# Kernel optimization log

Hardware: AMD Instinct MI355X
Metric: run time of the kernel (lower is better)

## Reference

```python
import jax, jax.numpy as jnp
import numpy as np

BS, SEQ, H = 8, 2048, 1024   # batch, tokens, hidden (longformer-large)
NSP = 32                     # discourse spans per essay
NH, HD = 16, 64              # attention heads, head dim
MAXPOS = 512                 # BertConfig default max_position_embeddings
NLAB = 3                     # effectiveness classes
EPS = 1e-5
SCALE = float(1.0 / np.sqrt(HD))


def _layer_norm(x, g, b):
    m = jnp.mean(x, -1, keepdims=True)
    v = jnp.var(x, -1, keepdims=True)
    return (x - m) * jax.lax.rsqrt(v + EPS) * g + b


def _lstm_dir(x, Wih, Whh, b, reverse):
    # x: [B,T,D] -> [B,T,Hh]; PyTorch gate order i,f,g,o
    pre = jnp.swapaxes(x, 0, 1) @ Wih.T + b  # [T,B,4Hh] input projection precomputed
    Hh = Whh.shape[1]
    z = jnp.zeros((x.shape[0], Hh), x.dtype)

    def step(carry, p):
        h, c = carry
        gates = p + h @ Whh.T
        i, f, g, o = jnp.split(gates, 4, axis=-1)
        c = jax.nn.sigmoid(f) * c + jax.nn.sigmoid(i) * jnp.tanh(g)
        h = jax.nn.sigmoid(o) * jnp.tanh(c)
        return (h, c), h

    _, ys = jax.lax.scan(step, (z, z), pre, reverse=reverse)
    return jnp.swapaxes(ys, 0, 1)


def _forward(span_head_idxs, span_tail_idxs, encoder_layer, span_attention_mask,
             lstm_Wih_f, lstm_Whh_f, lstm_b_f, lstm_Wih_b, lstm_Whh_b, lstm_b_b,
             ln_g, ln_b, Wq, bq, Wk, bk, Wv, bv, dist_emb, Wo, bo, ao_g, ao_b, Wc, bc):
    # BiLSTM over token features
    fwd = _lstm_dir(encoder_layer, lstm_Wih_f, lstm_Whh_f, lstm_b_f, False)
    bwd = _lstm_dir(encoder_layer, lstm_Wih_b, lstm_Whh_b, lstm_b_b, True)
    seq = jnp.concatenate([fwd, bwd], -1)  # [B,S,H]
    # ragged span mean pooling over tokens in (head, tail) (head excluded)
    pos = jnp.arange(SEQ)
    m = ((pos[None, None, :] > span_head_idxs[:, :, None]) &
         (pos[None, None, :] < span_tail_idxs[:, :, None])).astype(seq.dtype)  # [B,N,S]
    cnt = jnp.sum(m, -1, keepdims=True)
    mean_vec = jnp.einsum('bns,bsd->bnd', m, seq) / cnt
    x = _layer_norm(mean_vec, ln_g, ln_b)  # [B,N,H]
    # relative-key BertAttention over spans
    sh = lambda t: jnp.swapaxes(t.reshape(BS, NSP, NH, HD), 1, 2)  # [B,NH,N,HD]
    q, k, v = sh(x @ Wq + bq), sh(x @ Wk + bk), sh(x @ Wv + bv)
    scores = jnp.einsum('bhqd,bhkd->bhqk', q, k)
    dist = jnp.arange(NSP)[:, None] - jnp.arange(NSP)[None, :] + MAXPOS - 1
    pe = dist_emb[dist]  # [N,N,HD]
    scores = (scores + jnp.einsum('bhld,lrd->bhlr', q, pe)) * SCALE
    amask = (1.0 - span_attention_mask)[:, None, None, :] * -10000.0
    probs = jax.nn.softmax(scores + amask, axis=-1)
    ctx = jnp.swapaxes(jnp.einsum('bhqk,bhkd->bhqd', probs, v), 1, 2).reshape(BS, NSP, H)
    attn_out = _layer_norm(ctx @ Wo + bo + x, ao_g, ao_b)  # BertSelfOutput residual LN
    return attn_out @ Wc + bc  # logits [B,N,NLAB]


def setup_inputs():
    key = jax.random.key(0)
    ks = jax.random.split(key, 16)
    s, Hh = 0.02, H // 2
    span_len = SEQ // NSP
    heads = jnp.tile(jnp.arange(NSP) * span_len, (BS, 1)).astype(jnp.int32)
    f32 = jnp.float32
    return dict(
        encoder_layer=jax.random.normal(ks[0], (BS, SEQ, H), f32),
        span_head_idxs=heads,
        span_tail_idxs=heads + span_len,
        span_attention_mask=jnp.ones((BS, NSP), f32),
        lstm_Wih_f=jax.random.normal(ks[1], (4 * Hh, H), f32) * s,
        lstm_Whh_f=jax.random.normal(ks[2], (4 * Hh, Hh), f32) * s,
        lstm_b_f=jnp.zeros((4 * Hh,), f32),
        lstm_Wih_b=jax.random.normal(ks[3], (4 * Hh, H), f32) * s,
        lstm_Whh_b=jax.random.normal(ks[4], (4 * Hh, Hh), f32) * s,
        lstm_b_b=jnp.zeros((4 * Hh,), f32),
        ln_g=jnp.ones((H,), f32), ln_b=jnp.zeros((H,), f32),
        Wq=jax.random.normal(ks[5], (H, H), f32) * s, bq=jnp.zeros((H,), f32),
        Wk=jax.random.normal(ks[6], (H, H), f32) * s, bk=jnp.zeros((H,), f32),
        Wv=jax.random.normal(ks[7], (H, H), f32) * s, bv=jnp.zeros((H,), f32),
        dist_emb=jax.random.normal(ks[8], (2 * MAXPOS - 1, HD), f32) * s,
        Wo=jax.random.normal(ks[9], (H, H), f32) * s, bo=jnp.zeros((H,), f32),
        ao_g=jnp.ones((H,), f32), ao_b=jnp.zeros((H,), f32),
        Wc=jax.random.normal(ks[10], (H, NLAB), f32) * s, bc=jnp.zeros((NLAB,), f32),
    )


def reference(encoder_layer, span_head_idxs, span_tail_idxs, span_attention_mask,
              lstm_Wih_f, lstm_Whh_f, lstm_b_f, lstm_Wih_b, lstm_Whh_b, lstm_b_b,
              ln_g, ln_b, Wq, bq, Wk, bk, Wv, bv, dist_emb, Wo, bo, ao_g, ao_b, Wc, bc):
    return _forward(span_head_idxs, span_tail_idxs, encoder_layer, span_attention_mask,
                    lstm_Wih_f, lstm_Whh_f, lstm_b_f, lstm_Wih_b, lstm_Whh_b, lstm_b_b,
                    ln_g, ln_b, Wq, bq, Wk, bk, Wv, bv, dist_emb, Wo, bo, ao_g, ao_b, Wc, bc)
```

## Files before the change

kernel.cpp:

```cpp
#include <hip/hip_runtime.h>
#include <hip/hip_bf16.h>

#define BSZ   8
#define SEQL  2048
#define HID   1024
#define HH    512
#define NSP   32
#define NHEAD 16
#define HDIM  64

__device__ __forceinline__ float bf2f(unsigned short u) {
    unsigned int x = ((unsigned int)u) << 16;
    return __uint_as_float(x);
}
__device__ __forceinline__ unsigned short f2bf(float f) {
    unsigned int x = __float_as_uint(f);
    unsigned int r = (x + 0x7fffu + ((x >> 16) & 1u)) >> 16;
    return (unsigned short)r;
}

__device__ __forceinline__ void ldcg4x4(const float* p0, const float* p1,
                                        const float* p2, const float* p3,
                                        float4& a, float4& b, float4& c, float4& d) {
    asm volatile(
        "global_load_dwordx4 %0, %4, off sc0 sc1\n"
        "global_load_dwordx4 %1, %5, off sc0 sc1\n"
        "global_load_dwordx4 %2, %6, off sc0 sc1\n"
        "global_load_dwordx4 %3, %7, off sc0 sc1\n"
        "s_waitcnt vmcnt(0)"
        : "=&v"(a), "=&v"(b), "=&v"(c), "=&v"(d)
        : "v"(p0), "v"(p1), "v"(p2), "v"(p3)
        : "memory");
}
__device__ __forceinline__ void stcg_wait(float* p, float v) {
    asm volatile("global_store_dword %0, %1, off sc0 sc1\n"
                 "s_waitcnt vmcnt(0)"
                 :: "v"(p), "v"(v) : "memory");
}
__device__ __forceinline__ void stcg_i(int* p, int v) {
    asm volatile("global_store_dword %0, %1, off sc0 sc1"
                 :: "v"(p), "v"(v) : "memory");
}
__device__ __forceinline__ int ldcg_i(const int* p) {
    int v;
    asm volatile("global_load_dword %0, %1, off sc0 sc1\n"
                 "s_waitcnt vmcnt(0)"
                 : "=&v"(v) : "v"(p) : "memory");
    return v;
}

template<int TB, int OUTBF16, int PERM>
__global__ __launch_bounds__(256)
void gemm_f32(const float* __restrict__ X, const float* __restrict__ W,
              const float* __restrict__ bias, void* __restrict__ out,
              int M, int N, int K)
{
    __shared__ float a_s[16][132];
    __shared__ float b_s[16][132];
    const int tid = threadIdx.x;
    const int n0 = blockIdx.x * 128;
    const int m0 = blockIdx.y * 128;
    const int tx = tid & 15, ty = tid >> 4;
    float acc[8][8];
#pragma unroll
    for (int i = 0; i < 8; i++)
#pragma unroll
        for (int j = 0; j < 8; j++) acc[i][j] = 0.f;

    for (int k0 = 0; k0 < K; k0 += 16) {
#pragma unroll
        for (int i = 0; i < 2; i++) {
            int f4 = tid + 256 * i;
            int row = f4 >> 2, kc = f4 & 3;
            float4 v = *(const float4*)(X + (size_t)(m0 + row) * K + (k0 + kc * 4));
            a_s[kc*4+0][row] = v.x; a_s[kc*4+1][row] = v.y;
            a_s[kc*4+2][row] = v.z; a_s[kc*4+3][row] = v.w;
        }
        if (TB) {
#pragma unroll
            for (int i = 0; i < 2; i++) {
                int f4 = tid + 256 * i;
                int col = f4 >> 2, kc = f4 & 3;
                float4 v = *(const float4*)(W + (size_t)(n0 + col) * K + (k0 + kc * 4));
                b_s[kc*4+0][col] = v.x; b_s[kc*4+1][col] = v.y;
                b_s[kc*4+2][col] = v.z; b_s[kc*4+3][col] = v.w;
            }
        } else {
#pragma unroll
            for (int i = 0; i < 2; i++) {
                int f4 = tid + 256 * i;
                int kk = f4 >> 5, c4 = f4 & 31;
                float4 v = *(const float4*)(W + (size_t)(k0 + kk) * N + (n0 + c4 * 4));
                b_s[kk][c4*4+0] = v.x; b_s[kk][c4*4+1] = v.y;
                b_s[kk][c4*4+2] = v.z; b_s[kk][c4*4+3] = v.w;
            }
        }
        __syncthreads();
#pragma unroll
        for (int kk = 0; kk < 16; kk++) {
            float4 af0 = *(const float4*)&a_s[kk][ty * 8];
            float4 af1 = *(const float4*)&a_s[kk][ty * 8 + 4];
            float4 bf0 = *(const float4*)&b_s[kk][tx * 8];
            float4 bf1 = *(const float4*)&b_s[kk][tx * 8 + 4];
            float af[8] = {af0.x, af0.y, af0.z, af0.w, af1.x, af1.y, af1.z, af1.w};
            float bf[8] = {bf0.x, bf0.y, bf0.z, bf0.w, bf1.x, bf1.y, bf1.z, bf1.w};
#pragma unroll
            for (int i = 0; i < 8; i++)
#pragma unroll
                for (int j = 0; j < 8; j++)
                    acc[i][j] = fmaf(af[i], bf[j], acc[i][j]);
        }
        __syncthreads();
    }
#pragma unroll
    for (int i = 0; i < 8; i++) {
        int row = m0 + ty * 8 + i;
#pragma unroll
        for (int j = 0; j < 8; j++) {
            int col = n0 + tx * 8 + j;
            float v = acc[i][j] + bias[col];
            size_t oidx;
            if (PERM) {
                int bb = row >> 11; int tt = row & 2047;
                oidx = ((size_t)tt * 8 + bb) * (size_t)N + col;
            } else {
                oidx = (size_t)row * N + col;
            }
            if (OUTBF16) ((unsigned short*)out)[oidx] = f2bf(v);
            else         ((float*)out)[oidx] = v;
        }
    }
}

__global__ __launch_bounds__(256)
void lstm_rec_kernel(const unsigned short* __restrict__ pre_f,
                     const unsigned short* __restrict__ pre_b,
                     const float* __restrict__ Whh_f,
                     const float* __restrict__ Whh_b,
                     float* __restrict__ hbuf,
                     int* __restrict__ flags,
                     unsigned short* __restrict__ seq)
{
    const int tid = threadIdx.x;
    const int d = blockIdx.x >> 6;
    const int g = blockIdx.x & 63;
    const unsigned short* pre = d ? pre_b : pre_f;
    const float* Whh = d ? Whh_b : Whh_f;
    float* hb = hbuf + (size_t)d * 2 * 8 * 512;
    int* flg = flags + d * 64 * 32;
    int* myflag = flg + g * 32;

    __shared__ float h_s[4096];
    __shared__ float gate_s[8][33];

    const int m2 = tid >> 4;
    const int tk = tid & 15;
    float wA[32], wB[32];
    {
        const int mA = m2, mB = m2 + 16;
        const int growA = (mA >> 3) * 512 + g * 8 + (mA & 7);
        const int growB = (mB >> 3) * 512 + g * 8 + (mB & 7);
#pragma unroll
        for (int qq = 0; qq < 8; qq++) {
            float4 va = *(const float4*)(Whh + (size_t)growA * 512 + (qq * 16 + tk) * 4);
            float4 vb = *(const float4*)(Whh + (size_t)growB * 512 + (qq * 16 + tk) * 4);
            wA[qq*4+0] = va.x; wA[qq*4+1] = va.y; wA[qq*4+2] = va.z; wA[qq*4+3] = va.w;
            wB[qq*4+0] = vb.x; wB[qq*4+1] = vb.y; wB[qq*4+2] = vb.z; wB[qq*4+3] = vb.w;
        }
    }
    const int ub = tid >> 3;
    const int uj = tid & 7;
    const int ujj = g * 8 + uj;
    float cst = 0.f;

    for (int s = 0; s < 2048; s++) {
        const int t = d ? (2047 - s) : s;
        const float* hin = hb + (size_t)(s & 1) * 4096;
        float* hout = hb + (size_t)((s + 1) & 1) * 4096;

        float pv0 = 0.f, pv1 = 0.f, pv2 = 0.f, pv3 = 0.f;
        if (tid < 64) {
            const size_t pb = ((size_t)t * 8 + ub) * 2048;
            pv0 = bf2f(pre[pb + ujj]);
            pv1 = bf2f(pre[pb + 512 + ujj]);
            pv2 = bf2f(pre[pb + 1024 + ujj]);
            pv3 = bf2f(pre[pb + 1536 + ujj]);
        }

        if (tid < 64) {
            const int* fp = flg + tid * 32;
            int guard = 0;
            while (1) {
                int f = ldcg_i(fp);
                if (__all(f >= s)) break;
                if (++guard > (1 << 22)) break;
                __builtin_amdgcn_s_sleep(1);
            }
        }
        __syncthreads();

        {
            const float* base = hin + tid * 4;
            float4 va, vb2, vc, vd2;
            ldcg4x4(base, base + 1024, base + 2048, base + 3072, va, vb2, vc, vd2);
            float4* dst = (float4*)h_s;
            dst[tid] = va; dst[tid + 256] = vb2; dst[tid + 512] = vc; dst[tid + 768] = vd2;
        }
        __syncthreads();

#pragma unroll 1
        for (int b2 = 0; b2 < 8; b2++) {
            const float4* h4 = (const float4*)(h_s + b2 * 512);
            float s0 = 0.f, s1 = 0.f;
#pragma unroll
            for (int qq = 0; qq < 8; qq++) {
                float4 hv = h4[qq * 16 + tk];
                s0 += hv.x * wA[qq*4+0] + hv.y * wA[qq*4+1] + hv.z * wA[qq*4+2] + hv.w * wA[qq*4+3];
                s1 += hv.x * wB[qq*4+0] + hv.y * wB[qq*4+1] + hv.z * wB[qq*4+2] + hv.w * wB[qq*4+3];
            }
#pragma unroll
            for (int off = 1; off < 16; off <<= 1) {
                s0 += __shfl_xor(s0, off);
                s1 += __shfl_xor(s1, off);
            }
            if (tk == 0) { gate_s[b2][m2] = s0; gate_s[b2][m2 + 16] = s1; }
        }
        __syncthreads();

        if (tid < 64) {
            float zi = gate_s[ub][uj]      + pv0;
            float zf = gate_s[ub][8 + uj]  + pv1;
            float zg = gate_s[ub][16 + uj] + pv2;
            float zo = gate_s[ub][24 + uj] + pv3;
            float gi = 1.f / (1.f + __expf(-zi));
            float gf = 1.f / (1.f + __expf(-zf));
            float go = 1.f / (1.f + __expf(-zo));
            cst = gf * cst + gi * tanhf(zg);
            float hv = go * tanhf(cst);
            seq[((size_t)ub * 2048 + t) * 1024 + d * 512 + ujj] = f2bf(hv);
            stcg_wait(hout + ub * 512 + ujj, hv);
        }
        __syncthreads();
        if (tid == 0) stcg_i(myflag, s + 1);
    }
}

__global__ __launch_bounds__(256)
void pool_ln_kernel(const unsigned short* __restrict__ seq,
                    const int* __restrict__ heads, const int* __restrict__ tails,
                    const float* __restrict__ lng, const float* __restrict__ lnb,
                    float* __restrict__ xln)
{
    const int bn = blockIdx.x;
    const int b = bn >> 5;
    const int tid = threadIdx.x;
    const int head = heads[bn], tail = tails[bn];
    float a0 = 0.f, a1 = 0.f, a2 = 0.f, a3 = 0.f;
    for (int t = head + 1; t < tail; t++) {
        const unsigned short* p = seq + ((size_t)b * 2048 + t) * 1024 + tid * 4;
        uint2 w = *(const uint2*)p;
        a0 += bf2f((unsigned short)(w.x & 0xffff));
        a1 += bf2f((unsigned short)(w.x >> 16));
        a2 += bf2f((unsigned short)(w.y & 0xffff));
        a3 += bf2f((unsigned short)(w.y >> 16));
    }
    float cnt = (float)(tail - head - 1);
    float x0 = a0 / cnt, x1 = a1 / cnt, x2 = a2 / cnt, x3 = a3 / cnt;
    float s1 = x0 + x1 + x2 + x3;
    float s2 = x0*x0 + x1*x1 + x2*x2 + x3*x3;
#pragma unroll
    for (int off = 1; off < 64; off <<= 1) { s1 += __shfl_xor(s1, off); s2 += __shfl_xor(s2, off); }
    __shared__ float red[8];
    if ((tid & 63) == 0) { int w = tid >> 6; red[w] = s1; red[4 + w] = s2; }
    __syncthreads();
    s1 = red[0] + red[1] + red[2] + red[3];
    s2 = red[4] + red[5] + red[6] + red[7];
    float m = s1 * (1.f / 1024.f);
    float var = s2 * (1.f / 1024.f) - m * m;
    float inv = rsqrtf(var + 1e-5f);
    int c = tid * 4;
    float* o = xln + (size_t)bn * 1024 + c;
    o[0] = (x0 - m) * inv * lng[c+0] + lnb[c+0];
    o[1] = (x1 - m) * inv * lng[c+1] + lnb[c+1];
    o[2] = (x2 - m) * inv * lng[c+2] + lnb[c+2];
    o[3] = (x3 - m) * inv * lng[c+3] + lnb[c+3];
}

__global__ __launch_bounds__(256)
void attn_kernel(const float* __restrict__ q, const float* __restrict__ k,
                 const float* __restrict__ v, const float* __restrict__ dist_emb,
                 const float* __restrict__ mask, float* __restrict__ ctx)
{
    __shared__ float q_s[32][65], k_s[32][65], v_s[32][65];
    __shared__ float pe_s[63][65];
    __shared__ float p_s[32][33];
    __shared__ float mk[32];
    const int tid = threadIdx.x;
    const int b = blockIdx.x >> 4, h = blockIdx.x & 15;

    for (int i = tid; i < 32 * 16; i += 256) {
        int n = i >> 4, c = (i & 15) * 4;
        const size_t base = ((size_t)(b * 32 + n)) * 1024 + h * 64 + c;
        float4 qv = *(const float4*)(q + base);
        float4 kv = *(const float4*)(k + base);
        float4 vv = *(const float4*)(v + base);
        q_s[n][c] = qv.x; q_s[n][c+1] = qv.y; q_s[n][c+2] = qv.z; q_s[n][c+3] = qv.w;
        k_s[n][c] = kv.x; k_s[n][c+1] = kv.y; k_s[n][c+2] = kv.z; k_s[n][c+3] = kv.w;
        v_s[n][c] = vv.x; v_s[n][c+1] = vv.y; v_s[n][c+2] = vv.z; v_s[n][c+3] = vv.w;
    }
    for (int i = tid; i < 63 * 16; i += 256) {
        int x = i >> 4, c = (i & 15) * 4;
        float4 pv = *(const float4*)(dist_emb + (size_t)(480 + x) * 64 + c);
        pe_s[x][c] = pv.x; pe_s[x][c+1] = pv.y; pe_s[x][c+2] = pv.z; pe_s[x][c+3] = pv.w;
    }
    if (tid < 32) mk[tid] = mask[b * 32 + tid];
    __syncthreads();

#pragma unroll
    for (int pi = 0; pi < 4; pi++) {
        int p = tid + 256 * pi;
        int l = p >> 5, r = p & 31;
        const float* qr = q_s[l];
        const float* kr = k_s[r];
        const float* pr = pe_s[l - r + 31];
        float acc = 0.f;
#pragma unroll
        for (int dd = 0; dd < 64; dd++) acc = fmaf(qr[dd], kr[dd] + pr[dd], acc);
        p_s[l][r] = acc * 0.125f + (1.f - mk[r]) * (-10000.f);
    }
    __syncthreads();
    {
        int l = tid >> 3, c = tid & 7;
        float v0 = p_s[l][c], v1 = p_s[l][c+8], v2 = p_s[l][c+16], v3 = p_s[l][c+24];
        float mx = fmaxf(fmaxf(v0, v1), fmaxf(v2, v3));
#pragma unroll
        for (int off = 1; off < 8; off <<= 1) mx = fmaxf(mx, __shfl_xor(mx, off));
        float e0 = __expf(v0 - mx), e1 = __expf(v1 - mx), e2 = __expf(v2 - mx), e3 = __expf(v3 - mx);
        float sm = e0 + e1 + e2 + e3;
#pragma unroll
        for (int off = 1; off < 8; off <<= 1) sm += __shfl_xor(sm, off);
        float inv = 1.f / sm;
        p_s[l][c] = e0 * inv; p_s[l][c+8] = e1 * inv; p_s[l][c+16] = e2 * inv; p_s[l][c+24] = e3 * inv;
    }
    __syncthreads();
    {
        int l = tid >> 3, dg = tid & 7;
        float o[8] = {0, 0, 0, 0, 0, 0, 0, 0};
#pragma unroll 4
        for (int r = 0; r < 32; r++) {
            float pv = p_s[l][r];
#pragma unroll
            for (int j = 0; j < 8; j++) o[j] = fmaf(pv, v_s[r][dg * 8 + j], o[j]);
        }
        size_t base = ((size_t)(b * 32 + l)) * 1024 + h * 64 + dg * 8;
#pragma unroll
        for (int j = 0; j < 8; j++) ctx[base + j] = o[j];
    }
}

__global__ __launch_bounds__(256)
void resid_ln_kernel(const float* __restrict__ tmp, const float* __restrict__ xln,
                     const float* __restrict__ g, const float* __restrict__ be,
                     float* __restrict__ out)
{
    const int bn = blockIdx.x;
    const int tid = threadIdx.x;
    size_t base = (size_t)bn * 1024 + tid * 4;
    float4 a = *(const float4*)(tmp + base);
    float4 r = *(const float4*)(xln + base);
    float x0 = a.x + r.x, x1 = a.y + r.y, x2 = a.z + r.z, x3 = a.w + r.w;
    float s1 = x0 + x1 + x2 + x3;
    float s2 = x0*x0 + x1*x1 + x2*x2 + x3*x3;
#pragma unroll
    for (int off = 1; off < 64; off <<= 1) { s1 += __shfl_xor(s1, off); s2 += __shfl_xor(s2, off); }
    __shared__ float red[8];
    if ((tid & 63) == 0) { int w = tid >> 6; red[w] = s1; red[4 + w] = s2; }
    __syncthreads();
    s1 = red[0] + red[1] + red[2] + red[3];
    s2 = red[4] + red[5] + red[6] + red[7];
    float m = s1 * (1.f / 1024.f);
    float var = s2 * (1.f / 1024.f) - m * m;
    float inv = rsqrtf(var + 1e-5f);
    int c = tid * 4;
    out[base + 0] = (x0 - m) * inv * g[c+0] + be[c+0];
    out[base + 1] = (x1 - m) * inv * g[c+1] + be[c+1];
    out[base + 2] = (x2 - m) * inv * g[c+2] + be[c+2];
    out[base + 3] = (x3 - m) * inv * g[c+3] + be[c+3];
}

__global__ __launch_bounds__(256)
void classify_kernel(const float* __restrict__ x, const float* __restrict__ Wc,
                     const float* __restrict__ bc, float* __restrict__ out)
{
    const int bn = blockIdx.x;
    const int tid = threadIdx.x;
    const float* row = x + (size_t)bn * 1024;
    float a0 = 0.f, a1 = 0.f, a2 = 0.f;
    for (int kk = tid; kk < 1024; kk += 256) {
        float xv = row[kk];
        a0 = fmaf(xv, Wc[kk * 3 + 0], a0);
        a1 = fmaf(xv, Wc[kk * 3 + 1], a1);
        a2 = fmaf(xv, Wc[kk * 3 + 2], a2);
    }
#pragma unroll
    for (int off = 1; off < 64; off <<= 1) {
        a0 += __shfl_xor(a0, off); a1 += __shfl_xor(a1, off); a2 += __shfl_xor(a2, off);
    }
    __shared__ float red[12];
    if ((tid & 63) == 0) { int w = tid >> 6; red[w*3] = a0; red[w*3+1] = a1; red[w*3+2] = a2; }
    __syncthreads();
    if (tid == 0) {
        out[bn * 3 + 0] = red[0] + red[3] + red[6] + red[9]  + bc[0];
        out[bn * 3 + 1] = red[1] + red[4] + red[7] + red[10] + bc[1];
        out[bn * 3 + 2] = red[2] + red[5] + red[8] + red[11] + bc[2];
    }
}

#define OFF_PREF 0ull
#define OFF_PREB 67108864ull
#define OFF_SEQ  134217728ull
#define OFF_XLN  167772160ull
#define OFF_Q    168820736ull
#define OFF_K    169869312ull
#define OFF_V    170917888ull
#define OFF_CTX  171966464ull
#define OFF_TMP  173015040ull
#define OFF_ATT  174063616ull
#define OFF_HBUF 175112192ull
#define OFF_SYNC 175177728ull

extern "C" void kernel_launch(void* const* d_in, const int* in_sizes, int n_in,
                              void* d_out, int out_size, void* d_ws, size_t ws_size,
                              hipStream_t stream)
{
    const float* enc   = (const float*)d_in[0];
    const int*   heads = (const int*)d_in[1];
    const int*   tails = (const int*)d_in[2];
    const float* amask = (const float*)d_in[3];
    const float* Wih_f = (const float*)d_in[4];
    const float* Whh_f = (const float*)d_in[5];
    const float* b_f   = (const float*)d_in[6];
    const float* Wih_b = (const float*)d_in[7];
    const float* Whh_b = (const float*)d_in[8];
    const float* b_b   = (const float*)d_in[9];
    const float* ln_g  = (const float*)d_in[10];
    const float* ln_b  = (const float*)d_in[11];
    const float* Wq    = (const float*)d_in[12];
    const float* bq    = (const float*)d_in[13];
    const float* Wk    = (const float*)d_in[14];
    const float* bk    = (const float*)d_in[15];
    const float* Wv    = (const float*)d_in[16];
    const float* bv    = (const float*)d_in[17];
    const float* dist  = (const float*)d_in[18];
    const float* Wo    = (const float*)d_in[19];
    const float* bo    = (const float*)d_in[20];
    const float* ao_g  = (const float*)d_in[21];
    const float* ao_b  = (const float*)d_in[22];
    const float* Wc    = (const float*)d_in[23];
    const float* bc    = (const float*)d_in[24];

    char* ws = (char*)d_ws;
    unsigned short* pre_f = (unsigned short*)(ws + OFF_PREF);
    unsigned short* pre_b = (unsigned short*)(ws + OFF_PREB);
    unsigned short* seqp  = (unsigned short*)(ws + OFF_SEQ);
    float* xlnp = (float*)(ws + OFF_XLN);
    float* qb   = (float*)(ws + OFF_Q);
    float* kb   = (float*)(ws + OFF_K);
    float* vb   = (float*)(ws + OFF_V);
    float* ctxb = (float*)(ws + OFF_CTX);
    float* tmpb = (float*)(ws + OFF_TMP);
    float* attb = (float*)(ws + OFF_ATT);
    float* hbuf = (float*)(ws + OFF_HBUF);
    int*   flags = (int*)(ws + OFF_SYNC);

    hipMemsetAsync(ws + OFF_HBUF, 0, 65536 + 16384, stream);

    gemm_f32<1, 1, 1><<<dim3(16, 128), 256, 0, stream>>>(enc, Wih_f, b_f, pre_f, 16384, 2048, 1024);
    gemm_f32<1, 1, 1><<<dim3(16, 128), 256, 0, stream>>>(enc, Wih_b, b_b, pre_b, 16384, 2048, 1024);

    lstm_rec_kernel<<<128, 256, 0, stream>>>(pre_f, pre_b, Whh_f, Whh_b, hbuf, flags, seqp);

    pool_ln_kernel<<<256, 256, 0, stream>>>(seqp, heads, tails, ln_g, ln_b, xlnp);

    gemm_f32<0, 0, 0><<<dim3(8, 2), 256, 0, stream>>>(xlnp, Wq, bq, qb, 256, 1024, 1024);
    gemm_f32<0, 0, 0><<<dim3(8, 2), 256, 0, stream>>>(xlnp, Wk, bk, kb, 256, 1024, 1024);
    gemm_f32<0, 0, 0><<<dim3(8, 2), 256, 0, stream>>>(xlnp, Wv, bv, vb, 256, 1024, 1024);

    attn_kernel<<<128, 256, 0, stream>>>(qb, kb, vb, dist, amask, ctxb);

    gemm_f32<0, 0, 0><<<dim3(8, 2), 256, 0, stream>>>(ctxb, Wo, bo, tmpb, 256, 1024, 1024);
    resid_ln_kernel<<<256, 256, 0, stream>>>(tmpb, xlnp, ao_g, ao_b, attb);

    classify_kernel<<<256, 256, 0, stream>>>(attb, Wc, bc, (float*)d_out);
}
```

Before: 14.81 ms.

## Replicate LSTM hidden-state buffers and flags to spread cross-block polling traffic

The recurrent LSTM kernel now writes each step's hidden state and its progress flag to four replicas. Each block reads and polls only the replica chosen by its group index, so the 64 blocks per direction no longer all hit the same cache lines every step. The aim is to reduce contention on the global h-buffer and the flag lines in the per-step cross-block synchronisation. In exchange, each writer issues four times as many stores before its flag update, and the workspace offsets and memset size grow to hold the replicas.

```diff
diff --git a/kernel.cpp b/kernel.cpp
--- a/kernel.cpp
+++ b/kernel.cpp
@@ -8,6 +8,7 @@
 #define NSP   32
 #define NHEAD 16
 #define HDIM  64
+#define NREP  4
 
 __device__ __forceinline__ float bf2f(unsigned short u) {
     unsigned int x = ((unsigned int)u) << 16;
@@ -32,10 +33,15 @@
         : "v"(p0), "v"(p1), "v"(p2), "v"(p3)
         : "memory");
 }
-__device__ __forceinline__ void stcg_wait(float* p, float v) {
-    asm volatile("global_store_dword %0, %1, off sc0 sc1\n"
-                 "s_waitcnt vmcnt(0)"
-                 :: "v"(p), "v"(v) : "memory");
+__device__ __forceinline__ void stcg4_wait(float* p0, float* p1, float* p2,
+                                           float* p3, float v) {
+    asm volatile(
+        "global_store_dword %0, %4, off sc0 sc1\n"
+        "global_store_dword %1, %4, off sc0 sc1\n"
+        "global_store_dword %2, %4, off sc0 sc1\n"
+        "global_store_dword %3, %4, off sc0 sc1\n"
+        "s_waitcnt vmcnt(0)"
+        :: "v"(p0), "v"(p1), "v"(p2), "v"(p3), "v"(v) : "memory");
 }
 __device__ __forceinline__ void stcg_i(int* p, int v) {
     asm volatile("global_store_dword %0, %1, off sc0 sc1"
@@ -146,9 +152,9 @@
     const int g = blockIdx.x & 63;
     const unsigned short* pre = d ? pre_b : pre_f;
     const float* Whh = d ? Whh_b : Whh_f;
-    float* hb = hbuf + (size_t)d * 2 * 8 * 512;
-    int* flg = flags + d * 64 * 32;
-    int* myflag = flg + g * 32;
+    float* hb = hbuf + (size_t)d * 2 * NREP * 4096;
+    int* flg = flags + d * NREP * 64 * 32;
+    const int rsel = g & (NREP - 1);
 
     __shared__ float h_s[4096];
     __shared__ float gate_s[8][33];
@@ -175,8 +181,8 @@
 
     for (int s = 0; s < 2048; s++) {
         const int t = d ? (2047 - s) : s;
-        const float* hin = hb + (size_t)(s & 1) * 4096;
-        float* hout = hb + (size_t)((s + 1) & 1) * 4096;
+        const float* hin = hb + (size_t)(s & 1) * (NREP * 4096) + (size_t)rsel * 4096;
+        float* hout = hb + (size_t)((s + 1) & 1) * (NREP * 4096);
 
         float pv0 = 0.f, pv1 = 0.f, pv2 = 0.f, pv3 = 0.f;
         if (tid < 64) {
@@ -188,7 +194,7 @@
         }
 
         if (tid < 64) {
-            const int* fp = flg + tid * 32;
+            const int* fp = flg + rsel * (64 * 32) + tid * 32;
             int guard = 0;
             while (1) {
                 int f = ldcg_i(fp);
@@ -238,10 +244,15 @@
             cst = gf * cst + gi * tanhf(zg);
             float hv = go * tanhf(cst);
             seq[((size_t)ub * 2048 + t) * 1024 + d * 512 + ujj] = f2bf(hv);
-            stcg_wait(hout + ub * 512 + ujj, hv);
+            float* hp = hout + ub * 512 + ujj;
+            stcg4_wait(hp, hp + 4096, hp + 2 * 4096, hp + 3 * 4096, hv);
         }
         __syncthreads();
-        if (tid == 0) stcg_i(myflag, s + 1);
+        if (tid == 0) {
+#pragma unroll
+            for (int r = 0; r < NREP; r++)
+                stcg_i(flg + r * (64 * 32) + g * 32, s + 1);
+        }
     }
 }
 
@@ -427,7 +438,7 @@
 #define OFF_TMP  173015040ull
 #define OFF_ATT  174063616ull
 #define OFF_HBUF 175112192ull
-#define OFF_SYNC 175177728ull
+#define OFF_SYNC 175374336ull
 
 extern "C" void kernel_launch(void* const* d_in, const int* in_sizes, int n_in,
                               void* d_out, int out_size, void* d_ws, size_t ws_size,
@@ -473,7 +484,7 @@
     float* hbuf = (float*)(ws + OFF_HBUF);
     int*   flags = (int*)(ws + OFF_SYNC);
 
-    hipMemsetAsync(ws + OFF_HBUF, 0, 65536 + 16384, stream);
+    hipMemsetAsync(ws + OFF_HBUF, 0, 262144 + 65536, stream);
 
     gemm_f32<1, 1, 1><<<dim3(16, 128), 256, 0, stream>>>(enc, Wih_f, b_f, pre_f, 16384, 2048, 1024);
     gemm_f32<1, 1, 1><<<dim3(16, 128), 256, 0, stream>>>(enc, Wih_b, b_b, pre_b, 16384, 2048, 1024);
```

New measurement: 14.24 ms. 1.04x faster.
